# Performance work log

Measured on AMD Instinct MI355X. Metric: run time of the kernel, lower is better.

Reference implementation:

```python
import jax, jax.numpy as jnp
import numpy as np


def postorder_positions(depth):
    """Post-order index of each node in a perfect binary tree of given depth.
    Returns dict: level -> np.array of post-order indices for the left-to-right
    nodes at that level (level 0 = leaves, level `depth` = root)."""
    levels = {0: np.array([0], dtype=np.int64)}
    size = 1  # size of depth-(d-1) subtree
    for d in range(1, depth + 1):
        new = {l: np.concatenate([levels[l], levels[l] + size]) for l in range(d)}
        new[d] = np.array([2 * size], dtype=np.int64)
        levels = new
        size = 2 * size + 1
    return levels


def setup_inputs() -> dict:
    key = jax.random.key(0)
    k1, k2, k3, k4, k5, k6 = jax.random.split(key, 6)
    VOCAB, E, LBL, LEAVES = 50000, 100, 2, 131072  # 2**17 leaves
    word_ids = jax.random.randint(k1, (LEAVES,), 0, VOCAB, dtype=jnp.int32)
    emb_table = jax.random.normal(k2, (VOCAB, E), dtype=jnp.float32) * 0.1
    Wl = jax.random.normal(k3, (E, E), dtype=jnp.float32) * 0.1
    bl = jax.random.normal(k4, (E,), dtype=jnp.float32) * 0.1
    Wp = jax.random.normal(k5, (LBL, E), dtype=jnp.float32) * 0.1
    bp = jax.random.normal(k6, (LBL,), dtype=jnp.float32) * 0.1
    return {"word_ids": word_ids, "emb_table": emb_table, "Wl": Wl, "bl": bl, "Wp": Wp, "bp": bp}


def reference(word_ids, emb_table, Wl, bl, Wp, bp):
    # Perfect binary tree, batched level-by-level (same math as the per-node
    # Python recursion in the torch module). NOTE: original uses fcl for BOTH
    # children, so internal node = relu(fcl(left) + fcl(right)).
    L = word_ids.shape[0]
    D = int(round(np.log2(L)))
    pos = postorder_positions(D)
    n_nodes = 2 * L - 1

    h = emb_table[word_ids]  # [L, E] leaf states
    out = jnp.zeros((n_nodes, 1, bp.shape[0]), dtype=h.dtype)
    for lvl in range(D + 1):
        proj = h @ Wp.T + bp                     # [n_lvl, label]
        out = out.at[jnp.asarray(pos[lvl])].set(proj[:, None, :])
        if lvl < D:
            # fcl(left)+fcl(right) = (left+right) @ Wl^T + 2*bl, then relu
            h = jax.nn.relu((h[0::2] + h[1::2]) @ Wl.T + 2.0 * bl)
    return out  # [n_nodes, 1, label] in post-order, matching torch.cat(node_list)
```

## Files before the change

### kernel.cpp

```cpp
#include <hip/hip_runtime.h>

typedef _Float16 h8v __attribute__((ext_vector_type(8)));
typedef float f4v __attribute__((ext_vector_type(4)));

#define RS 136
#define SD 68

__device__ __forceinline__ unsigned pk2f(float a, float b) {
  unsigned short ha = __builtin_bit_cast(unsigned short, (_Float16)a);
  unsigned short hb = __builtin_bit_cast(unsigned short, (_Float16)b);
  return (unsigned)ha | ((unsigned)hb << 16);
}
__device__ __forceinline__ float2 upk(unsigned u) {
  _Float16 lo = __builtin_bit_cast(_Float16, (unsigned short)(u & 0xffffu));
  _Float16 hi = __builtin_bit_cast(_Float16, (unsigned short)(u >> 16));
  return make_float2((float)lo, (float)hi);
}

__global__ void prep_kernel(const float* __restrict__ Wl, const float* __restrict__ emb,
                            const float* __restrict__ Wp, const float* __restrict__ bp,
                            unsigned short* __restrict__ Wlf, unsigned* __restrict__ embh,
                            float2* __restrict__ pw) {
  const long t = (long)blockIdx.x * 256 + threadIdx.x;
  if (t < 100000L) {
    const int w = (int)(t >> 1), hh = (int)(t & 1);
    const float4* row4 = (const float4*)(emb + (size_t)w * 100);
    unsigned* ed = embh + (size_t)w * 64;
    float q0 = 0.f, q1 = 0.f;
    #pragma unroll
    for (int i = 0; i < 13; ++i) {
      int q = 13 * hh + i;
      if (q < 25) {
        float4 v = row4[q];
        q0 = fmaf(v.x, Wp[4*q], fmaf(v.y, Wp[4*q+1],
             fmaf(v.z, Wp[4*q+2], fmaf(v.w, Wp[4*q+3], q0))));
        q1 = fmaf(v.x, Wp[100+4*q], fmaf(v.y, Wp[100+4*q+1],
             fmaf(v.z, Wp[100+4*q+2], fmaf(v.w, Wp[100+4*q+3], q1))));
        ed[2*q]   = pk2f(v.x, v.y);
        ed[2*q+1] = pk2f(v.z, v.w);
      }
    }
    if (hh) {
      #pragma unroll
      for (int d = 50; d < 64; ++d) ed[d] = 0u;
    }
    q0 += __shfl_xor(q0, 1, 64);
    q1 += __shfl_xor(q1, 1, 64);
    if (!hh) pw[w] = make_float2(q0 + bp[0], q1 + bp[1]);
  } else {
    long j = t - 100096L;
    if (j >= 0 && j < 128 * 128) {
      int o = (int)(j >> 7), k = (int)(j & 127);
      _Float16 v = (_Float16)0.f;
      if (o < 100 && k < 100) v = (_Float16)Wl[o * 100 + k];
      Wlf[j] = __builtin_bit_cast(unsigned short, v);
    }
  }
}

__device__ __forceinline__ void load_bfrags(
    const unsigned short* __restrict__ Wlf, const float* __restrict__ bl,
    h8v (&B0)[4], h8v (&B1)[4], float& bias0, float& bias1,
    int wave, int quad, int c16) {
  int col0 = wave * 32 + c16;
  int col1 = col0 + 16;
  bias0 = (col0 < 100) ? 2.0f * bl[col0] : 0.f;
  bias1 = (col1 < 100) ? 2.0f * bl[col1] : 0.f;
  const _Float16* w0 = (const _Float16*)Wlf + col0 * 128 + quad * 8;
  const _Float16* w1 = (const _Float16*)Wlf + col1 * 128 + quad * 8;
  B0[0] = *(const h8v*)(w0);      B0[1] = *(const h8v*)(w0 + 32);
  B0[2] = *(const h8v*)(w0 + 64); B0[3] = *(const h8v*)(w0 + 96);
  B1[0] = *(const h8v*)(w1);      B1[1] = *(const h8v*)(w1 + 32);
  B1[2] = *(const h8v*)(w1 + 64); B1[3] = *(const h8v*)(w1 + 96);
}

__device__ __forceinline__ void mfma_level(
    const _Float16* srcE, const _Float16* srcO, bool pairMode,
    _Float16* dstE, _Float16* dstO, int nOut,
    const h8v (&B0)[4], const h8v (&B1)[4], float bias0, float bias1,
    int lane, int wave) {
  const int quad = lane >> 4, c16 = lane & 15;
  const int col0 = wave * 32 + c16, col1 = col0 + 16;
  const int tiles = (nOut + 15) >> 4;
  for (int rt = 0; rt < tiles; ++rt) {
    const int r = rt * 16 + c16;
    const h8v* pe = (const h8v*)(srcE + (size_t)r * RS + quad * 8);
    h8v A0, A1, A2, A3;
    if (pairMode) {
      const h8v* po = (const h8v*)(srcO + (size_t)r * RS + quad * 8);
      A0 = pe[0] + po[0];  A1 = pe[4] + po[4];
      A2 = pe[8] + po[8];  A3 = pe[12] + po[12];
    } else {
      A0 = pe[0]; A1 = pe[4]; A2 = pe[8]; A3 = pe[12];
    }
    f4v a0 = {bias0, bias0, bias0, bias0};
    f4v a1 = {bias1, bias1, bias1, bias1};
    a0 = __builtin_amdgcn_mfma_f32_16x16x32_f16(A0, B0[0], a0, 0, 0, 0);
    a0 = __builtin_amdgcn_mfma_f32_16x16x32_f16(A1, B0[1], a0, 0, 0, 0);
    a0 = __builtin_amdgcn_mfma_f32_16x16x32_f16(A2, B0[2], a0, 0, 0, 0);
    a0 = __builtin_amdgcn_mfma_f32_16x16x32_f16(A3, B0[3], a0, 0, 0, 0);
    a1 = __builtin_amdgcn_mfma_f32_16x16x32_f16(A0, B1[0], a1, 0, 0, 0);
    a1 = __builtin_amdgcn_mfma_f32_16x16x32_f16(A1, B1[1], a1, 0, 0, 0);
    a1 = __builtin_amdgcn_mfma_f32_16x16x32_f16(A2, B1[2], a1, 0, 0, 0);
    a1 = __builtin_amdgcn_mfma_f32_16x16x32_f16(A3, B1[3], a1, 0, 0, 0);
    #pragma unroll
    for (int rg = 0; rg < 4; ++rg) {
      int row = rt * 16 + quad * 4 + rg;
      _Float16* dr = ((row & 1) ? dstO : dstE) + (size_t)(row >> 1) * RS;
      dr[col0] = (_Float16)fmaxf(a0[rg], 0.f);
      dr[col1] = (_Float16)fmaxf(a1[rg], 0.f);
    }
  }
}

__device__ __forceinline__ void proj_rows(
    const _Float16* E, const _Float16* O, int nRows, const float* WpS,
    float bp0, float bp1, int lvl, long gbase, float* __restrict__ out, int tid) {
  if (tid >= nRows) return;
  const unsigned* row = (const unsigned*)((tid & 1) ? O : E) + (size_t)(tid >> 1) * SD;
  float q0 = bp0, q1 = bp1;
  #pragma unroll
  for (int p = 0; p < 25; ++p) {
    uint2 u = ((const uint2*)row)[p];
    float2 a = upk(u.x), b = upk(u.y);
    q0 = fmaf(a.x, WpS[4*p], fmaf(a.y, WpS[4*p+1],
         fmaf(b.x, WpS[4*p+2], fmaf(b.y, WpS[4*p+3], q0))));
    q1 = fmaf(a.x, WpS[128+4*p], fmaf(a.y, WpS[128+4*p+1],
         fmaf(b.x, WpS[128+4*p+2], fmaf(b.y, WpS[128+4*p+3], q1))));
  }
  long g = gbase + tid;
  long pos = ((g + 1) << (lvl + 1)) - 2 - __popc((unsigned)g);
  out[2 * pos] = q0; out[2 * pos + 1] = q1;
}

__device__ void tree_phase(
    const unsigned* __restrict__ src, unsigned* __restrict__ hdst,
    _Float16* Ea, _Float16* Oa, _Float16* Eb, _Float16* Ob,
    const float* WpS, float bp0, float bp1,
    const h8v (&B0)[4], const h8v (&B1)[4], float bias0, float bias1,
    float* __restrict__ out, int firstLvl, int nLvl, int nIn, int finalProj,
    long blk, int tid, int lane, int wave) {
  {
    unsigned* Ed = (unsigned*)Ea; unsigned* Od = (unsigned*)Oa;
    for (int i = tid; i < 64 * 64; i += 256) {
      int r = i >> 6, d = i & 63;
      unsigned val = (r < nIn && d < 50)
          ? __hip_atomic_load(&src[(size_t)r * 50 + d], __ATOMIC_RELAXED,
                              __HIP_MEMORY_SCOPE_AGENT)
          : 0u;
      ((r & 1) ? Od : Ed)[(r >> 1) * SD + d] = val;
    }
    unsigned* Ed2 = (unsigned*)Eb; unsigned* Od2 = (unsigned*)Ob;
    for (int i = tid; i < 32 * 64; i += 256) {
      int r = i >> 6, d = i & 63;
      ((r & 1) ? Od2 : Ed2)[(r >> 1) * SD + d] = 0u;
    }
  }
  __syncthreads();
  _Float16 *sE = Ea, *sO = Oa, *dE = Eb, *dO = Ob;
  int n = nIn >> 1;
  for (int p = 0; p < nLvl; ++p) {
    mfma_level(sE, sO, true, dE, dO, n, B0, B1, bias0, bias1, lane, wave);
    proj_rows(sE, sO, n * 2, WpS, bp0, bp1, firstLvl + p - 1,
              blk * (n * 2), out, tid);
    __syncthreads();
    _Float16* t;
    t = sE; sE = dE; dE = t;
    t = sO; sO = dO; dO = t;
    n >>= 1;
  }
  int R = nIn >> nLvl;
  if (finalProj)
    proj_rows(sE, sO, R, WpS, bp0, bp1, firstLvl + nLvl - 1, blk * R, out, tid);
  if (hdst) {
    for (int i = tid; i < R * 50; i += 256) {
      int r = i / 50, d = i % 50;
      unsigned val = ((const unsigned*)((r & 1) ? sO : sE))[(r >> 1) * SD + d];
      __hip_atomic_store(&hdst[(size_t)blk * R * 50 + i], val,
                         __ATOMIC_RELAXED, __HIP_MEMORY_SCOPE_AGENT);
    }
  }
  __syncthreads();
}

__global__ __launch_bounds__(256, 4) void mega_kernel(
    const int* __restrict__ word_ids, const unsigned* __restrict__ embh,
    const float2* __restrict__ pw,
    const unsigned short* __restrict__ Wlf, const float* __restrict__ bl,
    const float* __restrict__ Wp, const float* __restrict__ bp,
    unsigned* __restrict__ h7g, unsigned* __restrict__ h13g,
    unsigned* __restrict__ cnts, float* __restrict__ out) {
  __shared__ _Float16 S1[64 * RS];
  __shared__ _Float16 Ea[32 * RS], Oa[32 * RS];
  __shared__ float WpS[256];
  __shared__ int claimS;
  _Float16* const Eb = S1;
  _Float16* const Ob = S1 + 16 * RS;

  const int tid = threadIdx.x, lane = tid & 63;
  const int wave = __builtin_amdgcn_readfirstlane(tid >> 6);
  const int quad = lane >> 4, c16 = lane & 15;
  const int blk = blockIdx.x;

  {
    int r = tid >> 7, c = tid & 127;
    WpS[tid] = (c < 100) ? Wp[r * 100 + c] : 0.f;
  }
  const float bp0 = bp[0], bp1 = bp[1];

  const int l = tid >> 1, hh = tid & 1;
  const long gL = (long)blk * 128 + l;
  const int wid = word_ids[gL];
  const uint4* erow = (const uint4*)(embh + (size_t)wid * 64 + hh * 32);
  uint4 w4[8];
  #pragma unroll
  for (int i = 0; i < 8; ++i) w4[i] = erow[i];

  if (hh == 0) {
    float2 p = pw[wid];
    long pos = ((gL + 1) << 1) - 2 - __popc((unsigned)gL);
    out[2 * pos] = p.x; out[2 * pos + 1] = p.y;
  }

  {
    unsigned* S1d = (unsigned*)S1;
    const unsigned* wd = (const unsigned*)w4;
    #pragma unroll
    for (int k = 0; k < 32; ++k) {
      unsigned u = wd[k];
      unsigned us = __shfl_xor(u, 2, 64);
      float2 a = upk(u), b = upk(us);
      unsigned pk = pk2f(a.x + b.x, a.y + b.y);
      if ((tid & 2) == 0) S1d[(size_t)(tid >> 2) * SD + hh * 32 + k] = pk;
    }
  }
  h8v B0[4], B1[4]; float bias0, bias1;
  load_bfrags(Wlf, bl, B0, B1, bias0, bias1, wave, quad, c16);
  __syncthreads();

  mfma_level(S1, nullptr, false, Ea, Oa, 64, B0, B1, bias0, bias1, lane, wave);
  __syncthreads();
  mfma_level(Ea, Oa, true, Eb, Ob, 32, B0, B1, bias0, bias1, lane, wave);
  proj_rows(Ea, Oa, 64, WpS, bp0, bp1, 1, (long)blk * 64, out, tid);
  __syncthreads();
  mfma_level(Eb, Ob, true, Ea, Oa, 16, B0, B1, bias0, bias1, lane, wave);
  proj_rows(Eb, Ob, 32, WpS, bp0, bp1, 2, (long)blk * 32, out, tid);
  __syncthreads();
  mfma_level(Ea, Oa, true, Eb, Ob, 8, B0, B1, bias0, bias1, lane, wave);
  proj_rows(Ea, Oa, 16, WpS, bp0, bp1, 3, (long)blk * 16, out, tid);
  __syncthreads();
  mfma_level(Eb, Ob, true, Ea, Oa, 4, B0, B1, bias0, bias1, lane, wave);
  proj_rows(Eb, Ob, 8, WpS, bp0, bp1, 4, (long)blk * 8, out, tid);
  __syncthreads();
  mfma_level(Ea, Oa, true, Eb, Ob, 2, B0, B1, bias0, bias1, lane, wave);
  proj_rows(Ea, Oa, 4, WpS, bp0, bp1, 5, (long)blk * 4, out, tid);
  __syncthreads();
  mfma_level(Eb, Ob, true, Ea, Oa, 1, B0, B1, bias0, bias1, lane, wave);
  proj_rows(Eb, Ob, 2, WpS, bp0, bp1, 6, (long)blk * 2, out, tid);
  __syncthreads();
  if (tid < 50)
    __hip_atomic_store(&h7g[(size_t)blk * 50 + tid], ((unsigned*)Ea)[tid],
                       __ATOMIC_RELAXED, __HIP_MEMORY_SCOPE_AGENT);
  __syncthreads();

  const int g = blk >> 6;
  if (tid == 0) {
    unsigned old = __hip_atomic_fetch_add(&cnts[g], 1u, __ATOMIC_RELAXED,
                                          __HIP_MEMORY_SCOPE_AGENT);
    claimS = (old == 63u);
  }
  __syncthreads();
  if (!claimS) return;

  tree_phase(h7g + (size_t)g * 64 * 50, h13g, Ea, Oa, Eb, Ob, WpS, bp0, bp1,
             B0, B1, bias0, bias1, out, 8, 6, 64, 0, (long)g, tid, lane, wave);

  if (tid == 0) {
    unsigned old = __hip_atomic_fetch_add(&cnts[16], 1u, __ATOMIC_RELAXED,
                                          __HIP_MEMORY_SCOPE_AGENT);
    claimS = (old == 15u);
  }
  __syncthreads();
  if (!claimS) return;

  tree_phase(h13g, nullptr, Ea, Oa, Eb, Ob, WpS, bp0, bp1,
             B0, B1, bias0, bias1, out, 14, 4, 16, 1, 0L, tid, lane, wave);
}

extern "C" void kernel_launch(void* const* d_in, const int* in_sizes, int n_in,
                              void* d_out, int out_size, void* d_ws, size_t ws_size,
                              hipStream_t stream) {
  const int*   word_ids = (const int*)  d_in[0];
  const float* emb      = (const float*)d_in[1];
  const float* Wl       = (const float*)d_in[2];
  const float* bl       = (const float*)d_in[3];
  const float* Wp       = (const float*)d_in[4];
  const float* bp       = (const float*)d_in[5];
  float* out = (float*)d_out;

  unsigned*       embh = (unsigned*)d_ws;
  float2*         pw   = (float2*)((char*)d_ws + 12800000);
  unsigned short* Wlf  = (unsigned short*)((char*)d_ws + 13200000);
  unsigned*       h7g  = (unsigned*)((char*)d_ws + 13232768);
  unsigned*       h13g = (unsigned*)((char*)d_ws + 13437568);
  unsigned*       cnts = (unsigned*)((char*)d_ws + 13440768);

  hipMemsetAsync(cnts, 0, 128, stream);
  prep_kernel<<<455, 256, 0, stream>>>(Wl, emb, Wp, bp, Wlf, embh, pw);
  mega_kernel<<<1024, 256, 0, stream>>>(word_ids, embh, pw, Wlf, bl, Wp, bp,
                                        h7g, h13g, cnts, out);
}
```

Measured before the change: 153.6 us.

## Feed embedding rows straight into MFMA and defer projection stores

The first tree level now loads the four leaf embedding rows directly from global memory as MFMA A fragments. It sums the sibling pairs from the accumulator lanes, which removes the shuffle-based leaf-pair sum and the large LDS staging buffer. Per-level projection results are kept in registers and all output stores are issued at the end of each phase rather than between barriers. The tree_phase level count becomes a template parameter so its loops unroll, and the smaller LDS footprint may raise occupancy. In exchange, register pressure rises from the held projections and word ids, and the embedding loads are more scattered.

```diff
diff --git a/kernel.cpp b/kernel.cpp
--- a/kernel.cpp
+++ b/kernel.cpp
@@ -75,7 +75,7 @@
 }
 
 __device__ __forceinline__ void mfma_level(
-    const _Float16* srcE, const _Float16* srcO, bool pairMode,
+    const _Float16* srcE, const _Float16* srcO,
     _Float16* dstE, _Float16* dstO, int nOut,
     const h8v (&B0)[4], const h8v (&B1)[4], float bias0, float bias1,
     int lane, int wave) {
@@ -85,14 +85,9 @@
   for (int rt = 0; rt < tiles; ++rt) {
     const int r = rt * 16 + c16;
     const h8v* pe = (const h8v*)(srcE + (size_t)r * RS + quad * 8);
-    h8v A0, A1, A2, A3;
-    if (pairMode) {
-      const h8v* po = (const h8v*)(srcO + (size_t)r * RS + quad * 8);
-      A0 = pe[0] + po[0];  A1 = pe[4] + po[4];
-      A2 = pe[8] + po[8];  A3 = pe[12] + po[12];
-    } else {
-      A0 = pe[0]; A1 = pe[4]; A2 = pe[8]; A3 = pe[12];
-    }
+    const h8v* po = (const h8v*)(srcO + (size_t)r * RS + quad * 8);
+    h8v A0 = pe[0] + po[0], A1 = pe[4] + po[4];
+    h8v A2 = pe[8] + po[8], A3 = pe[12] + po[12];
     f4v a0 = {bias0, bias0, bias0, bias0};
     f4v a1 = {bias1, bias1, bias1, bias1};
     a0 = __builtin_amdgcn_mfma_f32_16x16x32_f16(A0, B0[0], a0, 0, 0, 0);
@@ -113,10 +108,9 @@
   }
 }
 
-__device__ __forceinline__ void proj_rows(
-    const _Float16* E, const _Float16* O, int nRows, const float* WpS,
-    float bp0, float bp1, int lvl, long gbase, float* __restrict__ out, int tid) {
-  if (tid >= nRows) return;
+__device__ __forceinline__ float2 proj_compute(
+    const _Float16* E, const _Float16* O, const float* WpS,
+    float bp0, float bp1, int tid) {
   const unsigned* row = (const unsigned*)((tid & 1) ? O : E) + (size_t)(tid >> 1) * SD;
   float q0 = bp0, q1 = bp1;
   #pragma unroll
@@ -128,18 +122,17 @@
     q1 = fmaf(a.x, WpS[128+4*p], fmaf(a.y, WpS[128+4*p+1],
          fmaf(b.x, WpS[128+4*p+2], fmaf(b.y, WpS[128+4*p+3], q1))));
   }
-  long g = gbase + tid;
-  long pos = ((g + 1) << (lvl + 1)) - 2 - __popc((unsigned)g);
-  out[2 * pos] = q0; out[2 * pos + 1] = q1;
-}
-
+  return make_float2(q0, q1);
+}
+
+template <int NLVL>
 __device__ void tree_phase(
     const unsigned* __restrict__ src, unsigned* __restrict__ hdst,
     _Float16* Ea, _Float16* Oa, _Float16* Eb, _Float16* Ob,
     const float* WpS, float bp0, float bp1,
     const h8v (&B0)[4], const h8v (&B1)[4], float bias0, float bias1,
-    float* __restrict__ out, int firstLvl, int nLvl, int nIn, int finalProj,
-    long blk, int tid, int lane, int wave) {
+    float* __restrict__ out, int firstLvl, int nIn, int finalProj,
+    long blkg, int tid, int lane, int wave) {
   {
     unsigned* Ed = (unsigned*)Ea; unsigned* Od = (unsigned*)Oa;
     for (int i = tid; i < 64 * 64; i += 256) {
@@ -157,28 +150,43 @@
     }
   }
   __syncthreads();
+  float2 tq[NLVL];
   _Float16 *sE = Ea, *sO = Oa, *dE = Eb, *dO = Ob;
   int n = nIn >> 1;
-  for (int p = 0; p < nLvl; ++p) {
-    mfma_level(sE, sO, true, dE, dO, n, B0, B1, bias0, bias1, lane, wave);
-    proj_rows(sE, sO, n * 2, WpS, bp0, bp1, firstLvl + p - 1,
-              blk * (n * 2), out, tid);
+  #pragma unroll
+  for (int p = 0; p < NLVL; ++p) {
+    mfma_level(sE, sO, dE, dO, n, B0, B1, bias0, bias1, lane, wave);
+    if (tid < 2 * n) tq[p] = proj_compute(sE, sO, WpS, bp0, bp1, tid);
     __syncthreads();
     _Float16* t;
     t = sE; sE = dE; dE = t;
     t = sO; sO = dO; dO = t;
     n >>= 1;
   }
-  int R = nIn >> nLvl;
-  if (finalProj)
-    proj_rows(sE, sO, R, WpS, bp0, bp1, firstLvl + nLvl - 1, blk * R, out, tid);
+  const int R = nIn >> NLVL;
+  float2 fq;
+  if (finalProj && tid < R) fq = proj_compute(sE, sO, WpS, bp0, bp1, tid);
   if (hdst) {
     for (int i = tid; i < R * 50; i += 256) {
       int r = i / 50, d = i % 50;
       unsigned val = ((const unsigned*)((r & 1) ? sO : sE))[(r >> 1) * SD + d];
-      __hip_atomic_store(&hdst[(size_t)blk * R * 50 + i], val,
+      __hip_atomic_store(&hdst[(size_t)blkg * R * 50 + i], val,
                          __ATOMIC_RELAXED, __HIP_MEMORY_SCOPE_AGENT);
     }
+  }
+  #pragma unroll
+  for (int p = 0; p < NLVL; ++p) {
+    int nR = nIn >> p;
+    if (tid < nR) {
+      long g = blkg * nR + tid;
+      long pos = ((g + 1) << (firstLvl + p)) - 2 - __popc((unsigned)g);
+      out[2 * pos] = tq[p].x; out[2 * pos + 1] = tq[p].y;
+    }
+  }
+  if (finalProj && tid < R) {
+    long g = blkg * R + tid;
+    long pos = ((g + 1) << (firstLvl + NLVL)) - 2 - __popc((unsigned)g);
+    out[2 * pos] = fq.x; out[2 * pos + 1] = fq.y;
   }
   __syncthreads();
 }
@@ -190,17 +198,24 @@
     const float* __restrict__ Wp, const float* __restrict__ bp,
     unsigned* __restrict__ h7g, unsigned* __restrict__ h13g,
     unsigned* __restrict__ cnts, float* __restrict__ out) {
-  __shared__ _Float16 S1[64 * RS];
   __shared__ _Float16 Ea[32 * RS], Oa[32 * RS];
+  __shared__ _Float16 Eb[16 * RS], Ob[16 * RS];
   __shared__ float WpS[256];
   __shared__ int claimS;
-  _Float16* const Eb = S1;
-  _Float16* const Ob = S1 + 16 * RS;
 
   const int tid = threadIdx.x, lane = tid & 63;
   const int wave = __builtin_amdgcn_readfirstlane(tid >> 6);
   const int quad = lane >> 4, c16 = lane & 15;
   const int blk = blockIdx.x;
+  const int col0 = wave * 32 + c16, col1 = col0 + 16;
+
+  int wid_r[8];
+  #pragma unroll
+  for (int rt = 0; rt < 8; ++rt)
+    wid_r[rt] = word_ids[(size_t)blk * 128 + rt * 16 + c16];
+
+  float2 p0 = make_float2(0.f, 0.f);
+  if (tid < 128) p0 = pw[word_ids[(size_t)blk * 128 + tid]];
 
   {
     int r = tid >> 7, c = tid & 127;
@@ -208,59 +223,68 @@
   }
   const float bp0 = bp[0], bp1 = bp[1];
 
-  const int l = tid >> 1, hh = tid & 1;
-  const long gL = (long)blk * 128 + l;
-  const int wid = word_ids[gL];
-  const uint4* erow = (const uint4*)(embh + (size_t)wid * 64 + hh * 32);
-  uint4 w4[8];
-  #pragma unroll
-  for (int i = 0; i < 8; ++i) w4[i] = erow[i];
-
-  if (hh == 0) {
-    float2 p = pw[wid];
-    long pos = ((gL + 1) << 1) - 2 - __popc((unsigned)gL);
-    out[2 * pos] = p.x; out[2 * pos + 1] = p.y;
-  }
-
-  {
-    unsigned* S1d = (unsigned*)S1;
-    const unsigned* wd = (const unsigned*)w4;
-    #pragma unroll
-    for (int k = 0; k < 32; ++k) {
-      unsigned u = wd[k];
-      unsigned us = __shfl_xor(u, 2, 64);
-      float2 a = upk(u), b = upk(us);
-      unsigned pk = pk2f(a.x + b.x, a.y + b.y);
-      if ((tid & 2) == 0) S1d[(size_t)(tid >> 2) * SD + hh * 32 + k] = pk;
-    }
-  }
   h8v B0[4], B1[4]; float bias0, bias1;
   load_bfrags(Wlf, bl, B0, B1, bias0, bias1, wave, quad, c16);
-  __syncthreads();
-
-  mfma_level(S1, nullptr, false, Ea, Oa, 64, B0, B1, bias0, bias1, lane, wave);
-  __syncthreads();
-  mfma_level(Ea, Oa, true, Eb, Ob, 32, B0, B1, bias0, bias1, lane, wave);
-  proj_rows(Ea, Oa, 64, WpS, bp0, bp1, 1, (long)blk * 64, out, tid);
-  __syncthreads();
-  mfma_level(Eb, Ob, true, Ea, Oa, 16, B0, B1, bias0, bias1, lane, wave);
-  proj_rows(Eb, Ob, 32, WpS, bp0, bp1, 2, (long)blk * 32, out, tid);
-  __syncthreads();
-  mfma_level(Ea, Oa, true, Eb, Ob, 8, B0, B1, bias0, bias1, lane, wave);
-  proj_rows(Ea, Oa, 16, WpS, bp0, bp1, 3, (long)blk * 16, out, tid);
-  __syncthreads();
-  mfma_level(Eb, Ob, true, Ea, Oa, 4, B0, B1, bias0, bias1, lane, wave);
-  proj_rows(Eb, Ob, 8, WpS, bp0, bp1, 4, (long)blk * 8, out, tid);
-  __syncthreads();
-  mfma_level(Ea, Oa, true, Eb, Ob, 2, B0, B1, bias0, bias1, lane, wave);
-  proj_rows(Ea, Oa, 4, WpS, bp0, bp1, 5, (long)blk * 4, out, tid);
-  __syncthreads();
-  mfma_level(Eb, Ob, true, Ea, Oa, 1, B0, B1, bias0, bias1, lane, wave);
-  proj_rows(Eb, Ob, 2, WpS, bp0, bp1, 6, (long)blk * 2, out, tid);
-  __syncthreads();
+
+  #pragma unroll
+  for (int rt = 0; rt < 8; ++rt) {
+    const h8v* ap = (const h8v*)(embh + (size_t)wid_r[rt] * 64 + quad * 4);
+    h8v A0 = ap[0], A1 = ap[4], A2 = ap[8], A3 = ap[12];
+    f4v a0 = {0.f, 0.f, 0.f, 0.f};
+    f4v a1 = {0.f, 0.f, 0.f, 0.f};
+    a0 = __builtin_amdgcn_mfma_f32_16x16x32_f16(A0, B0[0], a0, 0, 0, 0);
+    a0 = __builtin_amdgcn_mfma_f32_16x16x32_f16(A1, B0[1], a0, 0, 0, 0);
+    a0 = __builtin_amdgcn_mfma_f32_16x16x32_f16(A2, B0[2], a0, 0, 0, 0);
+    a0 = __builtin_amdgcn_mfma_f32_16x16x32_f16(A3, B0[3], a0, 0, 0, 0);
+    a1 = __builtin_amdgcn_mfma_f32_16x16x32_f16(A0, B1[0], a1, 0, 0, 0);
+    a1 = __builtin_amdgcn_mfma_f32_16x16x32_f16(A1, B1[1], a1, 0, 0, 0);
+    a1 = __builtin_amdgcn_mfma_f32_16x16x32_f16(A2, B1[2], a1, 0, 0, 0);
+    a1 = __builtin_amdgcn_mfma_f32_16x16x32_f16(A3, B1[3], a1, 0, 0, 0);
+    const int er = rt * 4 + quad;
+    Ea[(size_t)er * RS + col0] = (_Float16)fmaxf(a0[0] + a0[1] + bias0, 0.f);
+    Ea[(size_t)er * RS + col1] = (_Float16)fmaxf(a1[0] + a1[1] + bias1, 0.f);
+    Oa[(size_t)er * RS + col0] = (_Float16)fmaxf(a0[2] + a0[3] + bias0, 0.f);
+    Oa[(size_t)er * RS + col1] = (_Float16)fmaxf(a1[2] + a1[3] + bias1, 0.f);
+  }
+  __syncthreads();
+
+  float2 pq[6];
+  mfma_level(Ea, Oa, Eb, Ob, 32, B0, B1, bias0, bias1, lane, wave);
+  if (tid < 64) pq[0] = proj_compute(Ea, Oa, WpS, bp0, bp1, tid);
+  __syncthreads();
+  mfma_level(Eb, Ob, Ea, Oa, 16, B0, B1, bias0, bias1, lane, wave);
+  if (tid < 32) pq[1] = proj_compute(Eb, Ob, WpS, bp0, bp1, tid);
+  __syncthreads();
+  mfma_level(Ea, Oa, Eb, Ob, 8, B0, B1, bias0, bias1, lane, wave);
+  if (tid < 16) pq[2] = proj_compute(Ea, Oa, WpS, bp0, bp1, tid);
+  __syncthreads();
+  mfma_level(Eb, Ob, Ea, Oa, 4, B0, B1, bias0, bias1, lane, wave);
+  if (tid < 8) pq[3] = proj_compute(Eb, Ob, WpS, bp0, bp1, tid);
+  __syncthreads();
+  mfma_level(Ea, Oa, Eb, Ob, 2, B0, B1, bias0, bias1, lane, wave);
+  if (tid < 4) pq[4] = proj_compute(Ea, Oa, WpS, bp0, bp1, tid);
+  __syncthreads();
+  mfma_level(Eb, Ob, Ea, Oa, 1, B0, B1, bias0, bias1, lane, wave);
+  if (tid < 2) pq[5] = proj_compute(Eb, Ob, WpS, bp0, bp1, tid);
+  __syncthreads();
+
   if (tid < 50)
     __hip_atomic_store(&h7g[(size_t)blk * 50 + tid], ((unsigned*)Ea)[tid],
                        __ATOMIC_RELAXED, __HIP_MEMORY_SCOPE_AGENT);
+  if (tid < 128) {
+    long g = (long)blk * 128 + tid;
+    long pos = ((g + 1) << 1) - 2 - __popc((unsigned)g);
+    out[2 * pos] = p0.x; out[2 * pos + 1] = p0.y;
+  }
+  #pragma unroll
+  for (int L = 1; L <= 6; ++L) {
+    int nR = 128 >> L;
+    if (tid < nR) {
+      long g = (long)blk * nR + tid;
+      long pos = ((g + 1) << (L + 1)) - 2 - __popc((unsigned)g);
+      out[2 * pos] = pq[L - 1].x; out[2 * pos + 1] = pq[L - 1].y;
+    }
+  }
   __syncthreads();
 
   const int g = blk >> 6;
@@ -272,8 +296,8 @@
   __syncthreads();
   if (!claimS) return;
 
-  tree_phase(h7g + (size_t)g * 64 * 50, h13g, Ea, Oa, Eb, Ob, WpS, bp0, bp1,
-             B0, B1, bias0, bias1, out, 8, 6, 64, 0, (long)g, tid, lane, wave);
+  tree_phase<6>(h7g + (size_t)g * 64 * 50, h13g, Ea, Oa, Eb, Ob, WpS, bp0, bp1,
+                B0, B1, bias0, bias1, out, 8, 64, 0, (long)g, tid, lane, wave);
 
   if (tid == 0) {
     unsigned old = __hip_atomic_fetch_add(&cnts[16], 1u, __ATOMIC_RELAXED,
@@ -283,8 +307,8 @@
   __syncthreads();
   if (!claimS) return;
 
-  tree_phase(h13g, nullptr, Ea, Oa, Eb, Ob, WpS, bp0, bp1,
-             B0, B1, bias0, bias1, out, 14, 4, 16, 1, 0L, tid, lane, wave);
+  tree_phase<4>(h13g, nullptr, Ea, Oa, Eb, Ob, WpS, bp0, bp1,
+                B0, B1, bias0, bias1, out, 14, 16, 1, 0L, tid, lane, wave);
 }
 
 extern "C" void kernel_launch(void* const* d_in, const int* in_sizes, int n_in,
```

New measurement: 184.5 us. 20.1% more time.
